# Kernel optimization log

Hardware: AMD Instinct MI355X
Metric: run time of the kernel (lower is better)

Reference implementation:

```python
import jax, jax.numpy as jnp
import numpy as np

N_NODES = 100000


def setup_inputs() -> dict:
    key = jax.random.key(0)
    k1, k2, k3, k4 = jax.random.split(key, 4)
    d = 64
    E = 1200000
    x = jax.random.normal(k1, (N_NODES, d), dtype=jnp.float32)
    edge_index = jax.random.randint(k2, (2, E), 0, N_NODES, dtype=jnp.int64)
    # GraphConv(dim, 1): lin_rel (with bias) applied to aggregated neighbors,
    # lin_root (no bias) applied to self features.
    W_rel = jax.random.normal(k3, (d, 1), dtype=jnp.float32) / np.sqrt(d)
    b_rel = jnp.zeros((1,), dtype=jnp.float32)
    W_root = jax.random.normal(k4, (d, 1), dtype=jnp.float32) / np.sqrt(d)
    return {"x": x, "edge_index": edge_index, "W_rel": W_rel, "b_rel": b_rel, "W_root": W_root}


def reference(x, edge_index, W_rel, b_rel, W_root):
    # x: [N, d], edge_index: [2, E] (row 0 = source j, row 1 = target i)
    src, dst = edge_index[0], edge_index[1]
    # sum-aggregate neighbor features: agg[i] = sum_{j: (j,i) in E} x[j]
    agg = jax.ops.segment_sum(x[src], dst, num_segments=N_NODES)  # [N, d]
    # GraphConv: lin_rel(agg) + lin_root(x) -> scalar score per node
    attn = agg @ W_rel + b_rel + x @ W_root  # [N, 1]
    return attn
```

## Files before the change

kernel.cpp:

```cpp
#include <hip/hip_runtime.h>

#define DIM 64
#define NPB 256
#define NPB_SHIFT 8
#define THREADS 512
#define K2_U 8
#define K2_EPB (THREADS * K2_U)
#define STRIP K2_EPB
#define SRC_BITS 17
#define SRC_MASK ((1u << SRC_BITS) - 1u)
#define NODE_ROWS 128

__global__ __launch_bounds__(THREADS)
void fused_kernel(const float4* __restrict__ x4,
                  const float4* __restrict__ Wrel4,
                  const float* __restrict__ b_rel,
                  const float4* __restrict__ Wroot4,
                  const int* __restrict__ ei,
                  float* __restrict__ s,
                  float* __restrict__ out,
                  unsigned* __restrict__ bucket,
                  unsigned short* __restrict__ offs,
                  int E, int NB, int NBLK, int n) {
    __shared__ __align__(16) unsigned lpair[K2_EPB];
    __shared__ int  hist[THREADS];
    __shared__ int  wsum[8];

    int tid = threadIdx.x;

    if (blockIdx.x < NBLK) {
        int blk = blockIdx.x;
        hist[tid] = 0;
        __syncthreads();

        int base = blk * K2_EPB + tid * K2_U;
        int dst[K2_U], src[K2_U], rnk[K2_U], bin[K2_U];
        int have = 0;

        if (base + K2_U <= E) {
            const int4* sv = (const int4*)ei;
            const int4* dv = (const int4*)(ei + E);
            int g = base >> 2;
            int4 s0 = sv[g], s1 = sv[g + 1];
            int4 d0 = dv[g], d1 = dv[g + 1];
            src[0] = s0.x; src[1] = s0.y; src[2] = s0.z; src[3] = s0.w;
            src[4] = s1.x; src[5] = s1.y; src[6] = s1.z; src[7] = s1.w;
            dst[0] = d0.x; dst[1] = d0.y; dst[2] = d0.z; dst[3] = d0.w;
            dst[4] = d1.x; dst[5] = d1.y; dst[6] = d1.z; dst[7] = d1.w;
            have = K2_U;
        } else {
            #pragma unroll
            for (int k = 0; k < K2_U; ++k) {
                int e = base + k;
                if (e < E) {
                    src[k] = ei[e];
                    dst[k] = ei[E + e];
                    have = k + 1;
                }
            }
        }

        #pragma unroll
        for (int k = 0; k < K2_U; ++k) {
            if (k < have) {
                bin[k] = dst[k] >> NPB_SHIFT;
                rnk[k] = atomicAdd(&hist[bin[k]], 1);
            }
        }
        __syncthreads();

        int h = hist[tid];

        int lane = tid & 63;
        int w = tid >> 6;
        int incl = h;
        #pragma unroll
        for (int off = 1; off < 64; off <<= 1) {
            int v = __shfl_up(incl, off);
            if (lane >= off) incl += v;
        }
        if (lane == 63) wsum[w] = incl;
        __syncthreads();

        int wb = 0;
        #pragma unroll
        for (int i = 0; i < 8; ++i) wb += (i < w) ? wsum[i] : 0;
        int excl = wb + incl - h;

        if (tid <= NB)
            offs[(size_t)blk * (NB + 1) + tid] = (unsigned short)excl;

        hist[tid] = excl;
        __syncthreads();

        #pragma unroll
        for (int k = 0; k < K2_U; ++k) {
            if (k < have) {
                int slot = hist[bin[k]] + rnk[k];
                lpair[slot] = ((unsigned)(dst[k] & (NPB - 1)) << SRC_BITS)
                              | (unsigned)src[k];
            }
        }
        __syncthreads();

        int nE = min(K2_EPB, E - blk * K2_EPB);
        int n4 = (nE + 3) >> 2;
        const uint4* lp4 = (const uint4*)lpair;
        uint4* dp4 = (uint4*)(bucket + (size_t)blk * STRIP);
        for (int i = tid; i < n4; i += THREADS) dp4[i] = lp4[i];
    } else {
        int nb = blockIdx.x - NBLK;
        int lane16 = tid & 15;
        int rg = tid >> 4;
        int rowbase = nb * NODE_ROWS + rg;
        float4 wr = Wrel4[lane16];
        float4 wt = Wroot4[lane16];
        float b0 = b_rel[0];

        float4 xv[4];
        int row[4];
        #pragma unroll
        for (int k = 0; k < 4; ++k) {
            row[k] = rowbase + k * 32;
            xv[k] = (row[k] < n) ? x4[(size_t)row[k] * (DIM / 4) + lane16]
                                 : make_float4(0.f, 0.f, 0.f, 0.f);
        }
        #pragma unroll
        for (int k = 0; k < 4; ++k) {
            float sr = xv[k].x * wr.x + xv[k].y * wr.y
                     + xv[k].z * wr.z + xv[k].w * wr.w;
            float st = xv[k].x * wt.x + xv[k].y * wt.y
                     + xv[k].z * wt.z + xv[k].w * wt.w;
            #pragma unroll
            for (int off = 1; off < 16; off <<= 1) {
                sr += __shfl_xor(sr, off);
                st += __shfl_xor(st, off);
            }
            if (lane16 == 0 && row[k] < n) {
                s[row[k]]   = sr;
                out[row[k]] = st + b0;
            }
        }
    }
}

__global__ __launch_bounds__(THREADS)
void gather_kernel(const unsigned short* __restrict__ offs,
                   const unsigned* __restrict__ bucket,
                   const float* __restrict__ s,
                   float* __restrict__ out,
                   int NB, int NBLK, int n) {
    __shared__ float acc[NPB];
    int b = blockIdx.x;
    int tid = threadIdx.x;

    if (tid < NPB) acc[tid] = 0.f;
    __syncthreads();

    for (int strip = tid; strip < NBLK; strip += THREADS) {
        size_t ro = (size_t)strip * (NB + 1) + b;
        int o0 = offs[ro];
        int o1 = offs[ro + 1];
        const unsigned* sp = bucket + (size_t)strip * STRIP;
        for (int i = o0; i < o1; ++i) {
            unsigned p = sp[i];
            atomicAdd(&acc[p >> SRC_BITS], s[p & SRC_MASK]);
        }
    }
    __syncthreads();

    if (tid < NPB) {
        int g = b * NPB + tid;
        if (g < n) out[g] += acc[tid];
    }
}

extern "C" void kernel_launch(void* const* d_in, const int* in_sizes, int n_in,
                              void* d_out, int out_size, void* d_ws, size_t ws_size,
                              hipStream_t stream) {
    const float* x      = (const float*)d_in[0];
    const int*   ei     = (const int*)d_in[1];
    const float* W_rel  = (const float*)d_in[2];
    const float* b_rel  = (const float*)d_in[3];
    const float* W_root = (const float*)d_in[4];
    float* out = (float*)d_out;

    int n = out_size;
    int E = in_sizes[1] / 2;

    int NB   = (n + NPB - 1) / NPB;
    int NBLK = (E + K2_EPB - 1) / K2_EPB;

    float* s = (float*)d_ws;
    size_t off = ((size_t)n * 4 + 255) & ~(size_t)255;
    unsigned short* offs = (unsigned short*)((char*)d_ws + off);
    off += ((size_t)NBLK * (NB + 1) * 2 + 255) & ~(size_t)255;
    unsigned* bucket = (unsigned*)((char*)d_ws + off);

    int NODEBLKS = (n + NODE_ROWS - 1) / NODE_ROWS;
    fused_kernel<<<NBLK + NODEBLKS, THREADS, 0, stream>>>(
        (const float4*)x, (const float4*)W_rel, b_rel, (const float4*)W_root,
        ei, s, out, bucket, offs, E, NB, NBLK, n);

    gather_kernel<<<NB, THREADS, 0, stream>>>(offs, bucket, s, out, NB, NBLK, n);
}
```

Baseline: 31.97 us.

## Transpose bucket offset table, stage offsets in LDS, vectorize gather reads

Stores the per-strip bucket offsets transposed (bucket-major) so each gather block reads a contiguous row of offsets, which it stages into shared memory. The gather inner loop now loads packed pairs as uint4 with aligned head and tail loops, issuing four source-score loads before the LDS atomics. Node rows per block rise from 128 to 160, so fewer node blocks are launched. The gather now assumes NBLK <= THREADS (one strip per thread, no loop) and relies on uint4 alignment of the bucket strips.

```diff
diff --git a/kernel.cpp b/kernel.cpp
--- a/kernel.cpp
+++ b/kernel.cpp
@@ -9,7 +9,7 @@
 #define STRIP K2_EPB
 #define SRC_BITS 17
 #define SRC_MASK ((1u << SRC_BITS) - 1u)
-#define NODE_ROWS 128
+#define NODE_ROWS 160
 
 __global__ __launch_bounds__(THREADS)
 void fused_kernel(const float4* __restrict__ x4,
@@ -20,7 +20,7 @@
                   float* __restrict__ s,
                   float* __restrict__ out,
                   unsigned* __restrict__ bucket,
-                  unsigned short* __restrict__ offs,
+                  unsigned short* __restrict__ offsT,
                   int E, int NB, int NBLK, int n) {
     __shared__ __align__(16) unsigned lpair[K2_EPB];
     __shared__ int  hist[THREADS];
@@ -88,7 +88,7 @@
         int excl = wb + incl - h;
 
         if (tid <= NB)
-            offs[(size_t)blk * (NB + 1) + tid] = (unsigned short)excl;
+            offsT[(size_t)tid * NBLK + blk] = (unsigned short)excl;
 
         hist[tid] = excl;
         __syncthreads();
@@ -117,16 +117,16 @@
         float4 wt = Wroot4[lane16];
         float b0 = b_rel[0];
 
-        float4 xv[4];
-        int row[4];
-        #pragma unroll
-        for (int k = 0; k < 4; ++k) {
+        float4 xv[5];
+        int row[5];
+        #pragma unroll
+        for (int k = 0; k < 5; ++k) {
             row[k] = rowbase + k * 32;
             xv[k] = (row[k] < n) ? x4[(size_t)row[k] * (DIM / 4) + lane16]
                                  : make_float4(0.f, 0.f, 0.f, 0.f);
         }
         #pragma unroll
-        for (int k = 0; k < 4; ++k) {
+        for (int k = 0; k < 5; ++k) {
             float sr = xv[k].x * wr.x + xv[k].y * wr.y
                      + xv[k].z * wr.z + xv[k].w * wr.w;
             float st = xv[k].x * wt.x + xv[k].y * wt.y
@@ -145,24 +145,44 @@
 }
 
 __global__ __launch_bounds__(THREADS)
-void gather_kernel(const unsigned short* __restrict__ offs,
+void gather_kernel(const unsigned short* __restrict__ offsT,
                    const unsigned* __restrict__ bucket,
                    const float* __restrict__ s,
                    float* __restrict__ out,
                    int NB, int NBLK, int n) {
     __shared__ float acc[NPB];
+    __shared__ unsigned short o0s[THREADS], o1s[THREADS];
     int b = blockIdx.x;
     int tid = threadIdx.x;
 
     if (tid < NPB) acc[tid] = 0.f;
+    for (int t = tid; t < NBLK; t += THREADS) {
+        o0s[t] = offsT[(size_t)b * NBLK + t];
+        o1s[t] = offsT[(size_t)(b + 1) * NBLK + t];
+    }
     __syncthreads();
 
-    for (int strip = tid; strip < NBLK; strip += THREADS) {
-        size_t ro = (size_t)strip * (NB + 1) + b;
-        int o0 = offs[ro];
-        int o1 = offs[ro + 1];
-        const unsigned* sp = bucket + (size_t)strip * STRIP;
-        for (int i = o0; i < o1; ++i) {
+    if (tid < NBLK) {
+        int o0 = o0s[tid];
+        int o1 = o1s[tid];
+        const unsigned* sp = bucket + (size_t)tid * STRIP;
+        int i = o0;
+        for (; i < o1 && (i & 3); ++i) {
+            unsigned p = sp[i];
+            atomicAdd(&acc[p >> SRC_BITS], s[p & SRC_MASK]);
+        }
+        for (; i + 4 <= o1; i += 4) {
+            uint4 q = *(const uint4*)(sp + i);
+            float v0 = s[q.x & SRC_MASK];
+            float v1 = s[q.y & SRC_MASK];
+            float v2 = s[q.z & SRC_MASK];
+            float v3 = s[q.w & SRC_MASK];
+            atomicAdd(&acc[q.x >> SRC_BITS], v0);
+            atomicAdd(&acc[q.y >> SRC_BITS], v1);
+            atomicAdd(&acc[q.z >> SRC_BITS], v2);
+            atomicAdd(&acc[q.w >> SRC_BITS], v3);
+        }
+        for (; i < o1; ++i) {
             unsigned p = sp[i];
             atomicAdd(&acc[p >> SRC_BITS], s[p & SRC_MASK]);
         }
@@ -193,14 +213,14 @@
 
     float* s = (float*)d_ws;
     size_t off = ((size_t)n * 4 + 255) & ~(size_t)255;
-    unsigned short* offs = (unsigned short*)((char*)d_ws + off);
-    off += ((size_t)NBLK * (NB + 1) * 2 + 255) & ~(size_t)255;
+    unsigned short* offsT = (unsigned short*)((char*)d_ws + off);
+    off += ((size_t)(NB + 1) * NBLK * 2 + 255) & ~(size_t)255;
     unsigned* bucket = (unsigned*)((char*)d_ws + off);
 
     int NODEBLKS = (n + NODE_ROWS - 1) / NODE_ROWS;
     fused_kernel<<<NBLK + NODEBLKS, THREADS, 0, stream>>>(
         (const float4*)x, (const float4*)W_rel, b_rel, (const float4*)W_root,
-        ei, s, out, bucket, offs, E, NB, NBLK, n);
-
-    gather_kernel<<<NB, THREADS, 0, stream>>>(offs, bucket, s, out, NB, NBLK, n);
+        ei, s, out, bucket, offsT, E, NB, NBLK, n);
+
+    gather_kernel<<<NB, THREADS, 0, stream>>>(offsT, bucket, s, out, NB, NBLK, n);
 }
```

New measurement: 28.45 us, median of 2. 1.12x faster.
